# Optimization experiments

Hardware: AMD Instinct MI355X
Metric: run time of the kernel (lower is better)

The kernel has to match this reference:

```python
import jax, jax.numpy as jnp
import numpy as np

N_NODES = 32768   # 32 graphs x 1024 points
B_GRAPHS = 32
RATIO = 16
C_IN = 64
HEADS = 4
NEG_SLOPE = 0.2


def setup_inputs() -> dict:
    key = jax.random.key(0)
    ks = jax.random.split(key, 8)
    H, C = HEADS, C_IN
    x = jax.random.normal(ks[0], (N_NODES, C_IN), dtype=jnp.float32)
    edge_index = jax.random.randint(ks[1], (2, 1000), 0, N_NODES)  # ignored by forward
    batch = jnp.repeat(jnp.arange(B_GRAPHS), N_NODES // B_GRAPHS)  # sorted graph ids
    xcent_base = jax.random.normal(ks[2], (RATIO, C_IN), dtype=jnp.float32)
    s = 1.0 / np.sqrt(C_IN)
    W_l = jax.random.normal(ks[3], (C_IN, H * C), dtype=jnp.float32) * s
    b_l = jnp.zeros((H * C,), dtype=jnp.float32)
    W_r = jax.random.normal(ks[4], (C_IN, H * C), dtype=jnp.float32) * s
    b_r = jnp.zeros((H * C,), dtype=jnp.float32)
    att = jax.random.normal(ks[5], (H, C), dtype=jnp.float32) * s
    bias = jnp.zeros((C,), dtype=jnp.float32)
    return {"x": x, "edge_index": edge_index, "batch": batch,
            "xcent_base": xcent_base, "W_l": W_l, "b_l": b_l,
            "W_r": W_r, "b_r": b_r, "att": att, "bias": bias,
            "ratio": RATIO, "batch_size": B_GRAPHS}


def reference(x, edge_index, batch, xcent_base, W_l, b_l, W_r, b_r, att, bias,
              ratio, batch_size):
    # GATv2Conv bipartite: (x_src, x_dst=tiled xcent_base), concat=False (mean over heads)
    H, C = att.shape
    N = x.shape[0]
    T = batch_size * ratio                       # number of target centroids
    # edge list: each source node -> all `ratio` centroids of its graph
    src = jnp.repeat(jnp.arange(N), ratio)       # [E]
    tgt = jnp.tile(jnp.arange(ratio), N) + jnp.repeat(batch, ratio) * ratio  # [E]
    x_dst = jnp.tile(xcent_base, (batch_size, 1))          # [T, C_in]
    x_l = (x @ W_l + b_l).reshape(N, H, C)                 # source transform
    x_r = (x_dst @ W_r + b_r).reshape(T, H, C)             # target transform
    z = x_l[src] + x_r[tgt]                                # [E, H, C]
    z = jnp.where(z >= 0, z, NEG_SLOPE * z)                # LeakyReLU(0.2)
    logit = jnp.einsum('ehc,hc->eh', z, att)               # [E, H]
    # segment softmax over edges sharing a target centroid
    m = jax.ops.segment_max(logit, tgt, num_segments=T)
    ex = jnp.exp(logit - m[tgt])
    den = jax.ops.segment_sum(ex, tgt, num_segments=T)
    alpha = ex / den[tgt]                                  # [E, H]
    out = jax.ops.segment_sum(x_l[src] * alpha[:, :, None], tgt, num_segments=T)
    xcent = out.mean(axis=1) + bias                        # [T, C] (concat=False)
    batchcent = jnp.repeat(jnp.arange(batch_size), ratio)  # [T]
    return xcent, batchcent
```

## Files before the change

kernel.cpp:

```cpp
#include <hip/hip_runtime.h>


typedef __attribute__((ext_vector_type(8))) short short8;
typedef __attribute__((ext_vector_type(4))) float f32x4;

#define NPG 1024
#define NT 512

static __device__ __forceinline__ unsigned short f2bf(float f) {
    unsigned int u = __float_as_uint(f);
    u += 0x7fffu + ((u >> 16) & 1u);
    return (unsigned short)(u >> 16);
}
static __device__ __forceinline__ float bf2f(unsigned short u) {
    return __uint_as_float(((unsigned int)u) << 16);
}

__global__ __launch_bounds__(256) void k0_prep(const float* __restrict__ xcb,
                                               const float* __restrict__ W_l,
                                               const float* __restrict__ W_r,
                                               const float* __restrict__ b_r,
                                               const float* __restrict__ att,
                                               float* __restrict__ xrT,
                                               float* __restrict__ xr_att6,
                                               float* __restrict__ att6,
                                               float* __restrict__ att4,
                                               unsigned short* __restrict__ wt,
                                               float* __restrict__ out) {
    int b = blockIdx.x, t = threadIdx.x;
    if (b < 16) {
        int r = b, hc = t;
        float v = b_r[hc];
#pragma unroll
        for (int k = 0; k < 64; ++k)
            v = fmaf(xcb[r * 64 + k], W_r[k * 256 + hc], v);
        xrT[hc * 16 + r] = v;
        float p = 0.6f * att[hc] * v;
        p += __shfl_xor(p, 1);  p += __shfl_xor(p, 2);
        p += __shfl_xor(p, 4);  p += __shfl_xor(p, 8);
        p += __shfl_xor(p, 16); p += __shfl_xor(p, 32);
        if ((t & 63) == 0) xr_att6[r * 4 + (t >> 6)] = p;
    } else {
        att6[t] = 0.6f * att[t];
        att4[t] = 0.4f * att[t];
        unsigned short tmp[64] __attribute__((aligned(16)));
#pragma unroll
        for (int k = 0; k < 64; ++k) tmp[k] = f2bf(W_l[k * 256 + t]);
#pragma unroll
        for (int q = 0; q < 8; ++q)
            *(short8*)(wt + t * 64 + q * 8) = *(const short8*)(tmp + q * 8);
        out[NT * 64 + t]       = (float)(t >> 4);
        out[NT * 64 + 256 + t] = (float)((256 + t) >> 4);
    }
}

__global__ __launch_bounds__(256, 2) void k1_fused(const float* __restrict__ x,
                                                   const unsigned short* __restrict__ wt,
                                                   const float* __restrict__ b_l,
                                                   const float* __restrict__ att6,
                                                   const float* __restrict__ att4,
                                                   const float* __restrict__ xrT,
                                                   const float* __restrict__ xr_att6,
                                                   unsigned short* __restrict__ ws_pvh,
                                                   float* __restrict__ ws_denp) {
    __shared__ __align__(16) unsigned char smraw[(256 + 64) * 72 * 2];
    __shared__ __align__(16) float XR4[256][16];
    unsigned short (*As)[72]  = (unsigned short (*)[72])smraw;
    unsigned short (*xlT)[72] = (unsigned short (*)[72])smraw;
    unsigned short (*exT)[72] = (unsigned short (*)[72])(smraw + 256 * 72 * 2);

    const int t = threadIdx.x;
    const int blk = blockIdx.x;
    const int n0 = blk * 64;

    {
        int n = t >> 2, q = (t & 3) * 16;
        const float* p = x + (size_t)(n0 + n) * 64 + q;
        float4 v0 = *(const float4*)p;
        float4 v1 = *(const float4*)(p + 4);
        float4 v2 = *(const float4*)(p + 8);
        float4 v3 = *(const float4*)(p + 12);
        unsigned short h16[16] __attribute__((aligned(16)));
        h16[0]=f2bf(v0.x); h16[1]=f2bf(v0.y); h16[2]=f2bf(v0.z); h16[3]=f2bf(v0.w);
        h16[4]=f2bf(v1.x); h16[5]=f2bf(v1.y); h16[6]=f2bf(v1.z); h16[7]=f2bf(v1.w);
        h16[8]=f2bf(v2.x); h16[9]=f2bf(v2.y); h16[10]=f2bf(v2.z); h16[11]=f2bf(v2.w);
        h16[12]=f2bf(v3.x); h16[13]=f2bf(v3.y); h16[14]=f2bf(v3.z); h16[15]=f2bf(v3.w);
        *(short8*)(&As[n][q])     = *(const short8*)h16;
        *(short8*)(&As[n][q + 8]) = *(const short8*)(h16 + 8);
        const float4* xr = (const float4*)(xrT + t * 16);
        float4 r0 = xr[0], r1 = xr[1], r2 = xr[2], r3 = xr[3];
        float4* xd = (float4*)(&XR4[t][0]);
        xd[0] = r0; xd[1] = r1; xd[2] = r2; xd[3] = r3;
    }
    __syncthreads();

    const int l = t & 63;
    const int h = __builtin_amdgcn_readfirstlane(t >> 6);
    const int lm = l & 15, lq = l >> 4;
    const int lk = lq * 8;

    short8 af[4][2], bfr[4][2];
#pragma unroll
    for (int mt = 0; mt < 4; ++mt)
#pragma unroll
        for (int ks = 0; ks < 2; ++ks)
            af[mt][ks] = *(const short8*)(&As[mt * 16 + lm][ks * 32 + lk]);
#pragma unroll
    for (int nt = 0; nt < 4; ++nt)
#pragma unroll
        for (int ks = 0; ks < 2; ++ks)
            bfr[nt][ks] = *(const short8*)(wt + (size_t)(h * 64 + nt * 16 + lm) * 64 + ks * 32 + lk);

    f32x4 acc[4][4];
#pragma unroll
    for (int mt = 0; mt < 4; ++mt)
#pragma unroll
        for (int nt = 0; nt < 4; ++nt) { f32x4 z = {0.f,0.f,0.f,0.f}; acc[mt][nt] = z; }
#pragma unroll
    for (int mt = 0; mt < 4; ++mt)
#pragma unroll
        for (int nt = 0; nt < 4; ++nt)
#pragma unroll
            for (int ks = 0; ks < 2; ++ks)
                acc[mt][nt] = __builtin_amdgcn_mfma_f32_16x16x32_bf16(
                    af[mt][ks], bfr[nt][ks], acc[mt][nt], 0, 0, 0);

    __syncthreads();

#pragma unroll
    for (int nt = 0; nt < 4; ++nt) {
        float bl = b_l[h * 64 + nt * 16 + lm];
#pragma unroll
        for (int mt = 0; mt < 4; ++mt) {
            unsigned int d0 = (unsigned int)f2bf(acc[mt][nt][0] + bl) |
                              ((unsigned int)f2bf(acc[mt][nt][1] + bl) << 16);
            unsigned int d1 = (unsigned int)f2bf(acc[mt][nt][2] + bl) |
                              ((unsigned int)f2bf(acc[mt][nt][3] + bl) << 16);
            *(uint2*)(&xlT[h * 64 + nt * 16 + lm][mt * 16 + lq * 4]) = make_uint2(d0, d1);
        }
    }
    __syncthreads();

    float base = 0.f;
    float lacc[16];
#pragma unroll
    for (int r = 0; r < 16; ++r) lacc[r] = 0.f;
#pragma unroll 4
    for (int c = 0; c < 64; ++c) {
        int row = h * 64 + c;
        float xv = bf2f(xlT[row][l]);
        base = fmaf(xv, att6[row], base);
        float a4 = att4[row];
        float xr4v[16];
        const float4* xp = (const float4*)(&XR4[row][0]);
        *(float4*)(xr4v + 0)  = xp[0];
        *(float4*)(xr4v + 4)  = xp[1];
        *(float4*)(xr4v + 8)  = xp[2];
        *(float4*)(xr4v + 12) = xp[3];
#pragma unroll
        for (int r = 0; r < 16; ++r)
            lacc[r] = fmaf(fabsf(xv + xr4v[r]), a4, lacc[r]);
    }
#pragma unroll
    for (int r = 0; r < 16; ++r) {
        float ex = __expf(base + lacc[r] + xr_att6[r * 4 + h]);
        exT[h * 16 + r][l] = f2bf(ex);
    }
    __syncthreads();

    short8 ap[2];
#pragma unroll
    for (int ks = 0; ks < 2; ++ks)
        ap[ks] = *(const short8*)(&exT[h * 16 + lm][ks * 32 + lk]);
    short o = (lm == 0) ? (short)0x3F80 : (short)0;
    short8 onesf = {o, o, o, o, o, o, o, o};

    f32x4 pacc[4], dacc;
    { f32x4 z = {0.f,0.f,0.f,0.f}; pacc[0]=z; pacc[1]=z; pacc[2]=z; pacc[3]=z; dacc=z; }
#pragma unroll
    for (int ks = 0; ks < 2; ++ks) {
#pragma unroll
        for (int nt = 0; nt < 4; ++nt) {
            short8 bp = *(const short8*)(&xlT[h * 64 + nt * 16 + lm][ks * 32 + lk]);
            pacc[nt] = __builtin_amdgcn_mfma_f32_16x16x32_bf16(ap[ks], bp, pacc[nt], 0, 0, 0);
        }
        dacc = __builtin_amdgcn_mfma_f32_16x16x32_bf16(ap[ks], onesf, dacc, 0, 0, 0);
    }

    unsigned short* pvb = ws_pvh + ((size_t)blk * 4 + h) * 1024;
#pragma unroll
    for (int nt = 0; nt < 4; ++nt)
#pragma unroll
        for (int j = 0; j < 4; ++j)
            pvb[(lq * 4 + j) * 64 + nt * 16 + lm] = f2bf(pacc[nt][j]);
    if (lm == 0) {
#pragma unroll
        for (int j = 0; j < 4; ++j)
            ws_denp[((size_t)blk * 4 + h) * 16 + lq * 4 + j] = dacc[j];
    }
}

__global__ __launch_bounds__(256) void k2_final(const unsigned short* __restrict__ ws_pvh,
                                                const float* __restrict__ ws_denp,
                                                const float* __restrict__ bias,
                                                float* __restrict__ out) {
    int b = blockIdx.x;
    int g = b >> 2;
    int r = (b & 3) * 4 + (threadIdx.x >> 6);
    int c = threadIdx.x & 63;
    float acc = 0.f;
#pragma unroll
    for (int h = 0; h < 4; ++h) {
        float num = 0.f, den = 0.f;
#pragma unroll
        for (int tl = 0; tl < 16; ++tl) {
            num += bf2f(ws_pvh[(((size_t)(g * 16 + tl)) * 4 + h) * 1024 + r * 64 + c]);
            den += ws_denp[((size_t)(g * 16 + tl) * 4 + h) * 16 + r];
        }
        acc += num / den;
    }
    out[(size_t)(g * 16 + r) * 64 + c] = fmaf(0.25f, acc, bias[c]);
}

extern "C" void kernel_launch(void* const* d_in, const int* in_sizes, int n_in,
                              void* d_out, int out_size, void* d_ws, size_t ws_size,
                              hipStream_t stream) {
    const float* x    = (const float*)d_in[0];
    const float* xcb  = (const float*)d_in[3];
    const float* W_l  = (const float*)d_in[4];
    const float* b_l  = (const float*)d_in[5];
    const float* W_r  = (const float*)d_in[6];
    const float* b_r  = (const float*)d_in[7];
    const float* att  = (const float*)d_in[8];
    const float* bias = (const float*)d_in[9];
    float* out = (float*)d_out;

    unsigned short* ws_pvh = (unsigned short*)d_ws;
    float* ws_denp = (float*)(ws_pvh + 2097152);
    float* xrT     = ws_denp + 32768;
    float* xr_att6 = xrT + 4096;
    float* att6    = xr_att6 + 64;
    float* att4    = att6 + 256;
    unsigned short* wt = (unsigned short*)(att4 + 256);

    k0_prep<<<17, 256, 0, stream>>>(xcb, W_l, W_r, b_r, att, xrT, xr_att6, att6, att4, wt, out);
    k1_fused<<<512, 256, 0, stream>>>(x, wt, b_l, att6, att4, xrT, xr_att6, ws_pvh, ws_denp);
    k2_final<<<128, 256, 0, stream>>>(ws_pvh, ws_denp, bias, out);
}
```

Before: 31.46 us.

## Fold prep kernel into main kernel, recomputing target transform per block via MFMA

Removes the separate prep launch. Each block of the fused kernel now converts W_l and W_r from fp32 to bf16 itself and computes the centroid transform x_r with extra MFMAs, plus the attention projections it needs. The batchcent output writes move into two extra blocks of the final kernel, and the fp32-to-bf16 packing uses the v_cvt_pk_bf16_f32 instruction. This saves one kernel launch and its dependency, at the cost of redundant per-block weight loads, conversions and matmul work.

New measurement: 27.75 us. 1.13x faster.

```diff
diff --git a/kernel.cpp b/kernel.cpp
--- a/kernel.cpp
+++ b/kernel.cpp
@@ -15,59 +15,28 @@
 static __device__ __forceinline__ float bf2f(unsigned short u) {
     return __uint_as_float(((unsigned int)u) << 16);
 }
-
-__global__ __launch_bounds__(256) void k0_prep(const float* __restrict__ xcb,
-                                               const float* __restrict__ W_l,
-                                               const float* __restrict__ W_r,
-                                               const float* __restrict__ b_r,
-                                               const float* __restrict__ att,
-                                               float* __restrict__ xrT,
-                                               float* __restrict__ xr_att6,
-                                               float* __restrict__ att6,
-                                               float* __restrict__ att4,
-                                               unsigned short* __restrict__ wt,
-                                               float* __restrict__ out) {
-    int b = blockIdx.x, t = threadIdx.x;
-    if (b < 16) {
-        int r = b, hc = t;
-        float v = b_r[hc];
-#pragma unroll
-        for (int k = 0; k < 64; ++k)
-            v = fmaf(xcb[r * 64 + k], W_r[k * 256 + hc], v);
-        xrT[hc * 16 + r] = v;
-        float p = 0.6f * att[hc] * v;
-        p += __shfl_xor(p, 1);  p += __shfl_xor(p, 2);
-        p += __shfl_xor(p, 4);  p += __shfl_xor(p, 8);
-        p += __shfl_xor(p, 16); p += __shfl_xor(p, 32);
-        if ((t & 63) == 0) xr_att6[r * 4 + (t >> 6)] = p;
-    } else {
-        att6[t] = 0.6f * att[t];
-        att4[t] = 0.4f * att[t];
-        unsigned short tmp[64] __attribute__((aligned(16)));
-#pragma unroll
-        for (int k = 0; k < 64; ++k) tmp[k] = f2bf(W_l[k * 256 + t]);
-#pragma unroll
-        for (int q = 0; q < 8; ++q)
-            *(short8*)(wt + t * 64 + q * 8) = *(const short8*)(tmp + q * 8);
-        out[NT * 64 + t]       = (float)(t >> 4);
-        out[NT * 64 + 256 + t] = (float)((256 + t) >> 4);
-    }
+static __device__ __forceinline__ unsigned int cvt2(float a, float b) {
+    unsigned int r;
+    asm("v_cvt_pk_bf16_f32 %0, %1, %2" : "=v"(r) : "v"(a), "v"(b));
+    return r;
 }
 
 __global__ __launch_bounds__(256, 2) void k1_fused(const float* __restrict__ x,
-                                                   const unsigned short* __restrict__ wt,
+                                                   const float* __restrict__ W_l,
+                                                   const float* __restrict__ W_r,
                                                    const float* __restrict__ b_l,
-                                                   const float* __restrict__ att6,
-                                                   const float* __restrict__ att4,
-                                                   const float* __restrict__ xrT,
-                                                   const float* __restrict__ xr_att6,
+                                                   const float* __restrict__ b_r,
+                                                   const float* __restrict__ xcb,
+                                                   const float* __restrict__ att,
                                                    unsigned short* __restrict__ ws_pvh,
                                                    float* __restrict__ ws_denp) {
     __shared__ __align__(16) unsigned char smraw[(256 + 64) * 72 * 2];
     __shared__ __align__(16) float XR4[256][16];
+    __shared__ float SS[64];
     unsigned short (*As)[72]  = (unsigned short (*)[72])smraw;
     unsigned short (*xlT)[72] = (unsigned short (*)[72])smraw;
     unsigned short (*exT)[72] = (unsigned short (*)[72])(smraw + 256 * 72 * 2);
+    unsigned short (*XCB)[72] = exT;
 
     const int t = threadIdx.x;
     const int blk = blockIdx.x;
@@ -80,17 +49,17 @@
         float4 v1 = *(const float4*)(p + 4);
         float4 v2 = *(const float4*)(p + 8);
         float4 v3 = *(const float4*)(p + 12);
-        unsigned short h16[16] __attribute__((aligned(16)));
-        h16[0]=f2bf(v0.x); h16[1]=f2bf(v0.y); h16[2]=f2bf(v0.z); h16[3]=f2bf(v0.w);
-        h16[4]=f2bf(v1.x); h16[5]=f2bf(v1.y); h16[6]=f2bf(v1.z); h16[7]=f2bf(v1.w);
-        h16[8]=f2bf(v2.x); h16[9]=f2bf(v2.y); h16[10]=f2bf(v2.z); h16[11]=f2bf(v2.w);
-        h16[12]=f2bf(v3.x); h16[13]=f2bf(v3.y); h16[14]=f2bf(v3.z); h16[15]=f2bf(v3.w);
-        *(short8*)(&As[n][q])     = *(const short8*)h16;
-        *(short8*)(&As[n][q + 8]) = *(const short8*)(h16 + 8);
-        const float4* xr = (const float4*)(xrT + t * 16);
-        float4 r0 = xr[0], r1 = xr[1], r2 = xr[2], r3 = xr[3];
-        float4* xd = (float4*)(&XR4[t][0]);
-        xd[0] = r0; xd[1] = r1; xd[2] = r2; xd[3] = r3;
+        uint4 a, b;
+        a.x = cvt2(v0.x, v0.y); a.y = cvt2(v0.z, v0.w);
+        a.z = cvt2(v1.x, v1.y); a.w = cvt2(v1.z, v1.w);
+        b.x = cvt2(v2.x, v2.y); b.y = cvt2(v2.z, v2.w);
+        b.z = cvt2(v3.x, v3.y); b.w = cvt2(v3.z, v3.w);
+        *(uint4*)(&As[n][q])     = a;
+        *(uint4*)(&As[n][q + 8]) = b;
+        int rr = t >> 4, k4 = (t & 15) * 4;
+        float4 cv = *(const float4*)(xcb + rr * 64 + k4);
+        uint2 cw; cw.x = cvt2(cv.x, cv.y); cw.y = cvt2(cv.z, cv.w);
+        *(uint2*)(&XCB[rr][k4]) = cw;
     }
     __syncthreads();
 
@@ -99,23 +68,38 @@
     const int lm = l & 15, lq = l >> 4;
     const int lk = lq * 8;
 
-    short8 af[4][2], bfr[4][2];
+    short8 af[4][2], bfr[4][2], brf[4][2];
+#pragma unroll
+    for (int nt = 0; nt < 4; ++nt)
+#pragma unroll
+        for (int ks = 0; ks < 2; ++ks) {
+            const float* wl = W_l + (size_t)(ks * 32 + lk) * 256 + h * 64 + nt * 16 + lm;
+            const float* wr = W_r + (size_t)(ks * 32 + lk) * 256 + h * 64 + nt * 16 + lm;
+            uint4 pl, pr;
+            pl.x = cvt2(wl[0 * 256], wl[1 * 256]); pl.y = cvt2(wl[2 * 256], wl[3 * 256]);
+            pl.z = cvt2(wl[4 * 256], wl[5 * 256]); pl.w = cvt2(wl[6 * 256], wl[7 * 256]);
+            pr.x = cvt2(wr[0 * 256], wr[1 * 256]); pr.y = cvt2(wr[2 * 256], wr[3 * 256]);
+            pr.z = cvt2(wr[4 * 256], wr[5 * 256]); pr.w = cvt2(wr[6 * 256], wr[7 * 256]);
+            bfr[nt][ks] = *(short8*)&pl;
+            brf[nt][ks] = *(short8*)&pr;
+        }
 #pragma unroll
     for (int mt = 0; mt < 4; ++mt)
 #pragma unroll
         for (int ks = 0; ks < 2; ++ks)
             af[mt][ks] = *(const short8*)(&As[mt * 16 + lm][ks * 32 + lk]);
-#pragma unroll
-    for (int nt = 0; nt < 4; ++nt)
-#pragma unroll
-        for (int ks = 0; ks < 2; ++ks)
-            bfr[nt][ks] = *(const short8*)(wt + (size_t)(h * 64 + nt * 16 + lm) * 64 + ks * 32 + lk);
-
-    f32x4 acc[4][4];
+    short8 axc[2];
+#pragma unroll
+    for (int ks = 0; ks < 2; ++ks)
+        axc[ks] = *(const short8*)(&XCB[lm][ks * 32 + lk]);
+
+    f32x4 acc[4][4], axr[4];
 #pragma unroll
     for (int mt = 0; mt < 4; ++mt)
 #pragma unroll
         for (int nt = 0; nt < 4; ++nt) { f32x4 z = {0.f,0.f,0.f,0.f}; acc[mt][nt] = z; }
+#pragma unroll
+    for (int nt = 0; nt < 4; ++nt) { f32x4 z = {0.f,0.f,0.f,0.f}; axr[nt] = z; }
 #pragma unroll
     for (int mt = 0; mt < 4; ++mt)
 #pragma unroll
@@ -124,6 +108,12 @@
             for (int ks = 0; ks < 2; ++ks)
                 acc[mt][nt] = __builtin_amdgcn_mfma_f32_16x16x32_bf16(
                     af[mt][ks], bfr[nt][ks], acc[mt][nt], 0, 0, 0);
+#pragma unroll
+    for (int nt = 0; nt < 4; ++nt)
+#pragma unroll
+        for (int ks = 0; ks < 2; ++ks)
+            axr[nt] = __builtin_amdgcn_mfma_f32_16x16x32_bf16(
+                axc[ks], brf[nt][ks], axr[nt], 0, 0, 0);
 
     __syncthreads();
 
@@ -139,6 +129,34 @@
             *(uint2*)(&xlT[h * 64 + nt * 16 + lm][mt * 16 + lq * 4]) = make_uint2(d0, d1);
         }
     }
+    {
+        float brv[4], atw[4], pj[4];
+#pragma unroll
+        for (int nt = 0; nt < 4; ++nt) {
+            brv[nt] = b_r[h * 64 + nt * 16 + lm];
+            atw[nt] = att[h * 64 + nt * 16 + lm];
+        }
+#pragma unroll
+        for (int j = 0; j < 4; ++j) pj[j] = 0.f;
+#pragma unroll
+        for (int nt = 0; nt < 4; ++nt) {
+            float4 w;
+            w.x = axr[nt][0] + brv[nt]; w.y = axr[nt][1] + brv[nt];
+            w.z = axr[nt][2] + brv[nt]; w.w = axr[nt][3] + brv[nt];
+            *(float4*)(&XR4[h * 64 + nt * 16 + lm][lq * 4]) = w;
+            pj[0] = fmaf(w.x, atw[nt], pj[0]); pj[1] = fmaf(w.y, atw[nt], pj[1]);
+            pj[2] = fmaf(w.z, atw[nt], pj[2]); pj[3] = fmaf(w.w, atw[nt], pj[3]);
+        }
+#pragma unroll
+        for (int j = 0; j < 4; ++j) {
+            pj[j] += __shfl_xor(pj[j], 1); pj[j] += __shfl_xor(pj[j], 2);
+            pj[j] += __shfl_xor(pj[j], 4); pj[j] += __shfl_xor(pj[j], 8);
+        }
+        if (lm == 0) {
+#pragma unroll
+            for (int j = 0; j < 4; ++j) SS[h * 16 + lq * 4 + j] = 0.6f * pj[j];
+        }
+    }
     __syncthreads();
 
     float base = 0.f;
@@ -149,8 +167,9 @@
     for (int c = 0; c < 64; ++c) {
         int row = h * 64 + c;
         float xv = bf2f(xlT[row][l]);
-        base = fmaf(xv, att6[row], base);
-        float a4 = att4[row];
+        float attv = att[row];
+        base = fmaf(xv, attv, base);
+        float a4 = 0.4f * attv;
         float xr4v[16];
         const float4* xp = (const float4*)(&XR4[row][0]);
         *(float4*)(xr4v + 0)  = xp[0];
@@ -161,9 +180,10 @@
         for (int r = 0; r < 16; ++r)
             lacc[r] = fmaf(fabsf(xv + xr4v[r]), a4, lacc[r]);
     }
+    base *= 0.6f;
 #pragma unroll
     for (int r = 0; r < 16; ++r) {
-        float ex = __expf(base + lacc[r] + xr_att6[r * 4 + h]);
+        float ex = __expf(base + lacc[r] + SS[h * 16 + r]);
         exT[h * 16 + r][l] = f2bf(ex);
     }
     __syncthreads();
@@ -205,21 +225,26 @@
                                                 const float* __restrict__ bias,
                                                 float* __restrict__ out) {
     int b = blockIdx.x;
-    int g = b >> 2;
-    int r = (b & 3) * 4 + (threadIdx.x >> 6);
-    int c = threadIdx.x & 63;
-    float acc = 0.f;
-#pragma unroll
-    for (int h = 0; h < 4; ++h) {
-        float num = 0.f, den = 0.f;
-#pragma unroll
-        for (int tl = 0; tl < 16; ++tl) {
-            num += bf2f(ws_pvh[(((size_t)(g * 16 + tl)) * 4 + h) * 1024 + r * 64 + c]);
-            den += ws_denp[((size_t)(g * 16 + tl) * 4 + h) * 16 + r];
-        }
-        acc += num / den;
-    }
-    out[(size_t)(g * 16 + r) * 64 + c] = fmaf(0.25f, acc, bias[c]);
+    if (b < 128) {
+        int g = b >> 2;
+        int r = (b & 3) * 4 + (threadIdx.x >> 6);
+        int c = threadIdx.x & 63;
+        float acc = 0.f;
+#pragma unroll
+        for (int h = 0; h < 4; ++h) {
+            float num = 0.f, den = 0.f;
+#pragma unroll
+            for (int tl = 0; tl < 16; ++tl) {
+                num += bf2f(ws_pvh[(((size_t)(g * 16 + tl)) * 4 + h) * 1024 + r * 64 + c]);
+                den += ws_denp[((size_t)(g * 16 + tl) * 4 + h) * 16 + r];
+            }
+            acc += num / den;
+        }
+        out[(size_t)(g * 16 + r) * 64 + c] = fmaf(0.25f, acc, bias[c]);
+    } else {
+        int tt = (b - 128) * 256 + threadIdx.x;
+        out[NT * 64 + tt] = (float)(tt >> 4);
+    }
 }
 
 extern "C" void kernel_launch(void* const* d_in, const int* in_sizes, int n_in,
@@ -237,13 +262,7 @@
 
     unsigned short* ws_pvh = (unsigned short*)d_ws;
     float* ws_denp = (float*)(ws_pvh + 2097152);
-    float* xrT     = ws_denp + 32768;
-    float* xr_att6 = xrT + 4096;
-    float* att6    = xr_att6 + 64;
-    float* att4    = att6 + 256;
-    unsigned short* wt = (unsigned short*)(att4 + 256);
-
-    k0_prep<<<17, 256, 0, stream>>>(xcb, W_l, W_r, b_r, att, xrT, xr_att6, att6, att4, wt, out);
-    k1_fused<<<512, 256, 0, stream>>>(x, wt, b_l, att6, att4, xrT, xr_att6, ws_pvh, ws_denp);
-    k2_final<<<128, 256, 0, stream>>>(ws_pvh, ws_denp, bias, out);
-}
+
+    k1_fused<<<512, 256, 0, stream>>>(x, W_l, W_r, b_l, b_r, xcb, att, ws_pvh, ws_denp);
+    k2_final<<<130, 256, 0, stream>>>(ws_pvh, ws_denp, bias, out);
+}
```
